# Performance work log

Measured on AMD Instinct MI355X. Metric: run time of the kernel, lower is better.

The kernel has to match this reference:

```python
import jax, jax.numpy as jnp
import numpy as np

N, T, D = 512, 8, 64   # n_stocks, time_length, infeat
ALPHA, BETA = 0.5, 0.1


def setup_inputs() -> dict:
    key = jax.random.key(0)
    ks = jax.random.split(key, 5)
    x = jax.random.normal(ks[0], (N, T, D), jnp.float32)
    # RelationMapping params: fc1 (2D -> D), fc2 (D -> 1); stored as (in, out)
    W1 = jax.random.normal(ks[1], (2 * D, D), jnp.float32) * (1.0 / np.sqrt(2 * D))
    b1 = jnp.zeros((D,), jnp.float32)
    W2 = jax.random.normal(ks[2], (D, 1), jnp.float32) * (1.0 / np.sqrt(D))
    b2 = jnp.zeros((1,), jnp.float32)
    # time-attention parameter a: (T, 1), xavier-ish init
    a = jax.random.normal(ks[3], (T, 1), jnp.float32) * (1.414 * np.sqrt(2.0 / (T + 1)))
    return {"x": x, "W1": W1, "b1": b1, "W2": W2, "b2": b2, "a": a}


def reference(x, W1, b1, W2, b2, a):
    # x: (n, T, d). Original builds cat([x_i, x_j]) of shape (n, n, 2d) per
    # timestep; fc1(cat) decomposes exactly into x_i @ W1a + x_j @ W1b.
    n, t_len, d = x.shape
    W1a, W1b = W1[:d], W1[d:]               # (d, d) each
    L = jnp.einsum('ntd,dh->tnh', x, W1a)    # row (source) projection
    R = jnp.einsum('ntd,dh->tnh', x, W1b)    # col (target) projection
    w2 = W2[:, 0]                            # (d,)

    # time weights: softmax(a) * (1 + alpha * exp(-beta * (T - i - 1)))
    tt = jnp.arange(t_len, dtype=x.dtype)
    decay = 1.0 + ALPHA * jnp.exp(-BETA * (t_len - tt - 1.0))
    w = jax.nn.softmax(a[:, 0], axis=0) * decay  # (T,)

    def step(acc, args):
        Lt, Rt, wt = args
        h = jax.nn.relu(Lt[:, None, :] + Rt[None, :, :] + b1)  # (n, n, d)
        s = jax.nn.relu(h @ w2 + b2[0])                         # (n, n)
        return acc + wt * s, None

    A0 = jnp.zeros((n, n), x.dtype)
    A, _ = jax.lax.scan(step, A0, (L, R, w))
    return A
```

## Files before the change

kernel.cpp:

```cpp
#include <hip/hip_runtime.h>

#define NN 512
#define TT 8
#define DD 64

__global__ __launch_bounds__(256) void k1_proj(const float* __restrict__ x,
                                               const float* __restrict__ W1,
                                               const float* __restrict__ b1,
                                               float* __restrict__ L,
                                               float* __restrict__ R)
{
    int g    = blockIdx.x * 256 + threadIdx.x;
    int c    = g & 127;
    int h    = c & 63;
    int half = c >> 6;
    int pair = g >> 7;
    int n    = pair >> 1;
    int t0   = (pair & 1) * 4;

    float wcol[DD];
    const float* wbase = W1 + (half << 6) * DD + h;
#pragma unroll
    for (int d = 0; d < DD; ++d) wcol[d] = wbase[d << 6];

    float bias = half ? b1[h] : 0.0f;
    float* outbase = half ? R : L;

#pragma unroll
    for (int tt = 0; tt < 4; ++tt) {
        int t = t0 + tt;
        const float4* xr = (const float4*)(x + n * (TT * DD) + t * DD);
        float acc = 0.0f;
#pragma unroll
        for (int d4 = 0; d4 < 16; ++d4) {
            float4 xv = xr[d4];
            acc = fmaf(xv.x, wcol[d4 * 4 + 0], acc);
            acc = fmaf(xv.y, wcol[d4 * 4 + 1], acc);
            acc = fmaf(xv.z, wcol[d4 * 4 + 2], acc);
            acc = fmaf(xv.w, wcol[d4 * 4 + 3], acc);
        }
        outbase[t * (NN * DD) + n * DD + h] = acc + bias;
    }
}

__global__ __launch_bounds__(256) void k2_main(const float* __restrict__ L,
                                               const float* __restrict__ R,
                                               const float* __restrict__ W2,
                                               const float* __restrict__ b2,
                                               const float* __restrict__ a,
                                               float* __restrict__ A)
{
    __shared__ float Ls[2][32 * 64];
    __shared__ float Rs[2][32 * 64];
    __shared__ float w2s[64];
    __shared__ float wts[8];

    const int tid = threadIdx.x;
    const int i0  = blockIdx.y << 5;
    const int j0  = blockIdx.x << 5;
    const int tj  = tid & 15;
    const int ti  = tid >> 4;

    if (tid < 64) w2s[tid] = W2[tid];
    if (tid == 0) {
        float av[8], e[8];
        float m = -1e30f;
        for (int t = 0; t < 8; ++t) { av[t] = a[t]; m = fmaxf(m, av[t]); }
        float s = 0.0f;
        for (int t = 0; t < 8; ++t) { e[t] = expf(av[t] - m); s += e[t]; }
        for (int t = 0; t < 8; ++t)
            wts[t] = (e[t] / s) * (1.0f + 0.5f * expf(-0.1f * (float)(7 - t)));
    }

    const float b2v = b2[0];

    float4 lr0, lr1, rr0, rr1;
    auto stage_load = [&](int t) {
        const float4* lp = (const float4*)(L + t * (NN * DD) + i0 * DD);
        const float4* rp = (const float4*)(R + t * (NN * DD) + j0 * DD);
        lr0 = lp[tid]; lr1 = lp[tid + 256];
        rr0 = rp[tid]; rr1 = rp[tid + 256];
    };
    auto put = [&](float* base, int e, float4 v) {
        int row = e >> 4, col4 = e & 15;
        int pos = (row << 6) + ((col4 ^ ((row >> 1) & 7)) << 2);
        *(float4*)(base + pos) = v;
    };
    auto write_lds = [&](int buf) {
        put(Ls[buf], tid, lr0); put(Ls[buf], tid + 256, lr1);
        put(Rs[buf], tid, rr0); put(Rs[buf], tid + 256, rr1);
    };

    float acc00 = 0.f, acc01 = 0.f, acc10 = 0.f, acc11 = 0.f;
    const int riL0 = (2 * ti) << 6, riL1 = (2 * ti + 1) << 6;
    const int riR0 = (2 * tj) << 6, riR1 = (2 * tj + 1) << 6;
    const int swLb = ti & 7, swRb = tj & 7;

    stage_load(0);
    write_lds(0);
    stage_load(1);
    __syncthreads();

    for (int t = 0; t < 8; ++t) {
        const float* LB = Ls[t & 1];
        const float* RB = Rs[t & 1];
        float s00 = 0.f, s01 = 0.f, s10 = 0.f, s11 = 0.f;
#pragma unroll
        for (int d4 = 0; d4 < 16; ++d4) {
            const int swL = (d4 ^ swLb) << 2;
            const int swR = (d4 ^ swRb) << 2;
            float4 l0 = *(const float4*)(LB + riL0 + swL);
            float4 l1 = *(const float4*)(LB + riL1 + swL);
            float4 r0 = *(const float4*)(RB + riR0 + swR);
            float4 r1 = *(const float4*)(RB + riR1 + swR);
            float4 wv = *(const float4*)(w2s + (d4 << 2));
            s00 = fmaf(fmaxf(l0.x + r0.x, 0.f), wv.x, s00);
            s01 = fmaf(fmaxf(l0.x + r1.x, 0.f), wv.x, s01);
            s10 = fmaf(fmaxf(l1.x + r0.x, 0.f), wv.x, s10);
            s11 = fmaf(fmaxf(l1.x + r1.x, 0.f), wv.x, s11);
            s00 = fmaf(fmaxf(l0.y + r0.y, 0.f), wv.y, s00);
            s01 = fmaf(fmaxf(l0.y + r1.y, 0.f), wv.y, s01);
            s10 = fmaf(fmaxf(l1.y + r0.y, 0.f), wv.y, s10);
            s11 = fmaf(fmaxf(l1.y + r1.y, 0.f), wv.y, s11);
            s00 = fmaf(fmaxf(l0.z + r0.z, 0.f), wv.z, s00);
            s01 = fmaf(fmaxf(l0.z + r1.z, 0.f), wv.z, s01);
            s10 = fmaf(fmaxf(l1.z + r0.z, 0.f), wv.z, s10);
            s11 = fmaf(fmaxf(l1.z + r1.z, 0.f), wv.z, s11);
            s00 = fmaf(fmaxf(l0.w + r0.w, 0.f), wv.w, s00);
            s01 = fmaf(fmaxf(l0.w + r1.w, 0.f), wv.w, s01);
            s10 = fmaf(fmaxf(l1.w + r0.w, 0.f), wv.w, s10);
            s11 = fmaf(fmaxf(l1.w + r1.w, 0.f), wv.w, s11);
        }
        const float wt = wts[t];
        acc00 = fmaf(wt, fmaxf(s00 + b2v, 0.f), acc00);
        acc01 = fmaf(wt, fmaxf(s01 + b2v, 0.f), acc01);
        acc10 = fmaf(wt, fmaxf(s10 + b2v, 0.f), acc10);
        acc11 = fmaf(wt, fmaxf(s11 + b2v, 0.f), acc11);
        if (t < 7) {
            write_lds((t + 1) & 1);
            if (t + 2 < 8) stage_load(t + 2);
            __syncthreads();
        }
    }

    const int i = i0 + 2 * ti;
    const int j = j0 + 2 * tj;
    *(float2*)(A + i * NN + j)       = make_float2(acc00, acc01);
    *(float2*)(A + (i + 1) * NN + j) = make_float2(acc10, acc11);
}

extern "C" void kernel_launch(void* const* d_in, const int* in_sizes, int n_in,
                              void* d_out, int out_size, void* d_ws, size_t ws_size,
                              hipStream_t stream) {
    const float* x  = (const float*)d_in[0];
    const float* W1 = (const float*)d_in[1];
    const float* b1 = (const float*)d_in[2];
    const float* W2 = (const float*)d_in[3];
    const float* b2 = (const float*)d_in[4];
    const float* a  = (const float*)d_in[5];
    float* A = (float*)d_out;

    float* L = (float*)d_ws;
    float* R = L + NN * TT * DD;

    k1_proj<<<512, 256, 0, stream>>>(x, W1, b1, L, R);
    k2_main<<<dim3(16, 16), 256, 0, stream>>>(L, R, W2, b2, a, A);
}
```

Baseline: 93.81 us.

## Split timesteps across four thread groups per tile and reduce partials in LDS

The main kernel now runs 1024 threads per block. Each of four 256-thread groups handles two of the eight timesteps for the same 32x32 output tile. All L/R slices for the tile are loaded into about 128KB of dynamic LDS up front, which replaces the double-buffered per-timestep pipeline and its per-step barriers. Partial sums are then reduced through LDS. This gives each tile more parallelism across the 256 blocks on the GPU, at the cost of large LDS use that limits residency to one block per CU, plus an extra reduction step.

```diff
diff --git a/kernel.cpp b/kernel.cpp
--- a/kernel.cpp
+++ b/kernel.cpp
@@ -43,67 +43,73 @@
     }
 }
 
-__global__ __launch_bounds__(256) void k2_main(const float* __restrict__ L,
-                                               const float* __restrict__ R,
-                                               const float* __restrict__ W2,
-                                               const float* __restrict__ b2,
-                                               const float* __restrict__ a,
-                                               float* __restrict__ A)
+__global__ __launch_bounds__(1024, 4) void k2_main(const float* __restrict__ L,
+                                                   const float* __restrict__ R,
+                                                   const float* __restrict__ W2,
+                                                   const float* __restrict__ b2,
+                                                   const float* __restrict__ a,
+                                                   float* __restrict__ A)
 {
-    __shared__ float Ls[2][32 * 64];
-    __shared__ float Rs[2][32 * 64];
-    __shared__ float w2s[64];
-    __shared__ float wts[8];
+    extern __shared__ float S[];
+    float* const w2s = S + 32768;
 
     const int tid = threadIdx.x;
     const int i0  = blockIdx.y << 5;
     const int j0  = blockIdx.x << 5;
-    const int tj  = tid & 15;
-    const int ti  = tid >> 4;
 
+#pragma unroll
+    for (int k = 0; k < 8; ++k) {
+        int e    = tid + (k << 10);
+        int half = e >> 12;
+        int q    = e & 4095;
+        int t    = q >> 9;
+        int w    = q & 511;
+        int row  = w >> 4;
+        int c4   = w & 15;
+        const float* src = half ? (R + t * (NN * DD) + (j0 + row) * DD)
+                                : (L + t * (NN * DD) + (i0 + row) * DD);
+        float4 v = ((const float4*)src)[c4];
+        float* dst = S + (half ? 16384 : 0) + t * 2048 + (row << 6)
+                       + ((c4 ^ ((row >> 1) & 7)) << 2);
+        *(float4*)dst = v;
+    }
     if (tid < 64) w2s[tid] = W2[tid];
-    if (tid == 0) {
-        float av[8], e[8];
-        float m = -1e30f;
-        for (int t = 0; t < 8; ++t) { av[t] = a[t]; m = fmaxf(m, av[t]); }
-        float s = 0.0f;
-        for (int t = 0; t < 8; ++t) { e[t] = expf(av[t] - m); s += e[t]; }
-        for (int t = 0; t < 8; ++t)
-            wts[t] = (e[t] / s) * (1.0f + 0.5f * expf(-0.1f * (float)(7 - t)));
+
+    const int g  = tid >> 8;
+    const int id = tid & 255;
+    float wt0, wt1;
+    {
+        float av[8];
+#pragma unroll
+        for (int t = 0; t < 8; ++t) av[t] = a[t];
+        float m = av[0];
+#pragma unroll
+        for (int t = 1; t < 8; ++t) m = fmaxf(m, av[t]);
+        float ssum = 0.0f;
+#pragma unroll
+        for (int t = 0; t < 8; ++t) ssum += expf(av[t] - m);
+        float inv = 1.0f / ssum;
+        int ta = 2 * g, tb = 2 * g + 1;
+        wt0 = expf(av[ta] - m) * inv * (1.0f + 0.5f * expf(-0.1f * (float)(7 - ta)));
+        wt1 = expf(av[tb] - m) * inv * (1.0f + 0.5f * expf(-0.1f * (float)(7 - tb)));
     }
-
     const float b2v = b2[0];
 
-    float4 lr0, lr1, rr0, rr1;
-    auto stage_load = [&](int t) {
-        const float4* lp = (const float4*)(L + t * (NN * DD) + i0 * DD);
-        const float4* rp = (const float4*)(R + t * (NN * DD) + j0 * DD);
-        lr0 = lp[tid]; lr1 = lp[tid + 256];
-        rr0 = rp[tid]; rr1 = rp[tid + 256];
-    };
-    auto put = [&](float* base, int e, float4 v) {
-        int row = e >> 4, col4 = e & 15;
-        int pos = (row << 6) + ((col4 ^ ((row >> 1) & 7)) << 2);
-        *(float4*)(base + pos) = v;
-    };
-    auto write_lds = [&](int buf) {
-        put(Ls[buf], tid, lr0); put(Ls[buf], tid + 256, lr1);
-        put(Rs[buf], tid, rr0); put(Rs[buf], tid + 256, rr1);
-    };
+    __syncthreads();
+
+    const int tj = id & 15;
+    const int ti = id >> 4;
+    const int riL0 = (2 * ti) << 6,     riL1 = (2 * ti + 1) << 6;
+    const int riR0 = (2 * tj) << 6,     riR1 = (2 * tj + 1) << 6;
+    const int swLb = ti & 7,            swRb = tj & 7;
 
     float acc00 = 0.f, acc01 = 0.f, acc10 = 0.f, acc11 = 0.f;
-    const int riL0 = (2 * ti) << 6, riL1 = (2 * ti + 1) << 6;
-    const int riR0 = (2 * tj) << 6, riR1 = (2 * tj + 1) << 6;
-    const int swLb = ti & 7, swRb = tj & 7;
 
-    stage_load(0);
-    write_lds(0);
-    stage_load(1);
-    __syncthreads();
-
-    for (int t = 0; t < 8; ++t) {
-        const float* LB = Ls[t & 1];
-        const float* RB = Rs[t & 1];
+#pragma unroll
+    for (int tt = 0; tt < 2; ++tt) {
+        const int t = 2 * g + tt;
+        const float* LB = S + t * 2048;
+        const float* RB = S + 16384 + t * 2048;
         float s00 = 0.f, s01 = 0.f, s10 = 0.f, s11 = 0.f;
 #pragma unroll
         for (int d4 = 0; d4 < 16; ++d4) {
@@ -131,22 +137,29 @@
             s10 = fmaf(fmaxf(l1.w + r0.w, 0.f), wv.w, s10);
             s11 = fmaf(fmaxf(l1.w + r1.w, 0.f), wv.w, s11);
         }
-        const float wt = wts[t];
+        const float wt = tt ? wt1 : wt0;
         acc00 = fmaf(wt, fmaxf(s00 + b2v, 0.f), acc00);
         acc01 = fmaf(wt, fmaxf(s01 + b2v, 0.f), acc01);
         acc10 = fmaf(wt, fmaxf(s10 + b2v, 0.f), acc10);
         acc11 = fmaf(wt, fmaxf(s11 + b2v, 0.f), acc11);
-        if (t < 7) {
-            write_lds((t + 1) & 1);
-            if (t + 2 < 8) stage_load(t + 2);
-            __syncthreads();
-        }
     }
 
-    const int i = i0 + 2 * ti;
-    const int j = j0 + 2 * tj;
-    *(float2*)(A + i * NN + j)       = make_float2(acc00, acc01);
-    *(float2*)(A + (i + 1) * NN + j) = make_float2(acc10, acc11);
+    __syncthreads();
+    if (g > 0) {
+        ((float4*)S)[(g - 1) * 256 + id] = make_float4(acc00, acc01, acc10, acc11);
+    }
+    __syncthreads();
+    if (g == 0) {
+#pragma unroll
+        for (int gg = 0; gg < 3; ++gg) {
+            float4 p = ((const float4*)S)[gg * 256 + id];
+            acc00 += p.x; acc01 += p.y; acc10 += p.z; acc11 += p.w;
+        }
+        const int i = i0 + 2 * ti;
+        const int j = j0 + 2 * tj;
+        *(float2*)(A + i * NN + j)       = make_float2(acc00, acc01);
+        *(float2*)(A + (i + 1) * NN + j) = make_float2(acc10, acc11);
+    }
 }
 
 extern "C" void kernel_launch(void* const* d_in, const int* in_sizes, int n_in,
@@ -164,5 +177,7 @@
     float* R = L + NN * TT * DD;
 
     k1_proj<<<512, 256, 0, stream>>>(x, W1, b1, L, R);
-    k2_main<<<dim3(16, 16), 256, 0, stream>>>(L, R, W2, b2, a, A);
+
+    size_t ldsBytes = (32768 + 64) * sizeof(float);
+    k2_main<<<dim3(16, 16), 1024, ldsBytes, stream>>>(L, R, W2, b2, a, A);
 }
```

Measured after the change: 84.54 us. 1.11x faster.
